# Optimization experiments

Hardware: AMD Instinct MI355X
Metric: run time of the kernel (lower is better)

Reference implementation:

```python
import jax, jax.numpy as jnp
import numpy as np

N = 100000      # nodes
E = 1600000     # edges
F = 128         # num_node_features
C = 64          # graph_hidden_channels
NH = 256        # nhid
NOUT = 128      # nout
L = 4           # n_layers (hidden GCN layers)
G = 512         # number of graphs in batch


def setup_inputs() -> dict:
    key = jax.random.key(0)
    ks = jax.random.split(key, 10)
    x = jax.random.normal(ks[0], (N, F), jnp.float32)
    edge_index = jax.random.randint(ks[1], (2, E), 0, N, dtype=jnp.int64)
    batch = jnp.sort(jax.random.randint(ks[2], (N,), 0, G, dtype=jnp.int64))

    def w(k, shape, fan_in):
        return jax.random.normal(k, shape, jnp.float32) / np.float32(np.sqrt(fan_in))

    W0 = w(ks[3], (F, C), F)
    b0 = jnp.zeros((C,), jnp.float32)
    Wh = w(ks[4], (L, C, C), C)      # stacked hidden GCN weights
    bh = jnp.zeros((L, C), jnp.float32)
    W1 = w(ks[5], (C, NH), C)
    b1 = jnp.zeros((NH,), jnp.float32)
    W2 = w(ks[6], (NH, NOUT), NH)
    b2 = jnp.zeros((NOUT,), jnp.float32)
    return dict(x=x, edge_index=edge_index, batch=batch,
                W0=W0, b0=b0, Wh=Wh, bh=bh, W1=W1, b1=b1, W2=W2, b2=b2)


def _gcn_conv(h_in, W, b, src, dst, dinv):
    # PyG GCNConv: out_i = sum_{j->i} dinv_j * dinv_i * (x_j W) + dinv_i^2 * (x_i W) + b
    h = h_in @ W                                   # [N, C]
    coef = (dinv[src] * dinv[dst])[:, None]        # [E, 1]
    agg = jax.ops.segment_sum(h[src] * coef, dst, num_segments=N)
    agg = agg + h * (dinv * dinv)[:, None]         # self-loop term
    return agg + b


def reference(x, edge_index, batch, W0, b0, Wh, bh, W1, b1, W2, b2):
    src, dst = edge_index[0], edge_index[1]
    # degree with self loops (edge weight 1)
    deg = jax.ops.segment_sum(jnp.ones((E,), x.dtype), dst, num_segments=N) + 1.0
    dinv = jax.lax.rsqrt(deg)                      # [N]

    h = jax.nn.relu(_gcn_conv(x, W0, b0, src, dst, dinv))
    for i in range(L):
        h = jax.nn.relu(_gcn_conv(h, Wh[i], bh[i], src, dst, dinv))

    # global mean pool over graphs
    counts = jax.ops.segment_sum(jnp.ones((N,), x.dtype), batch, num_segments=G)
    pooled = jax.ops.segment_sum(h, batch, num_segments=G) / jnp.maximum(counts, 1.0)[:, None]

    out = jax.nn.relu(pooled @ W1 + b1)
    out = out @ W2 + b2
    return out
```

## Files before the change

kernel.cpp:

```cpp
#include <hip/hip_runtime.h>
#include <hip/hip_fp16.h>
#include <stddef.h>

static constexpr int Nn    = 100000;
static constexpr int Ee    = 1600000;
static constexpr int Ff    = 128;
static constexpr int Cc    = 64;
static constexpr int NHh   = 256;
static constexpr int NOUTt = 128;
static constexpr int Ll    = 4;
static constexpr int Gg    = 512;

static constexpr int SCAN_BLK = 1024;
static constexpr int NBLK_SCAN = (Nn + SCAN_BLK - 1) / SCAN_BLK;

static constexpr int NSUB   = (Nn + 511) / 512;
static constexpr int SUBCAP = 10240;

typedef _Float16 half8 __attribute__((ext_vector_type(8)));
typedef float    f32x4 __attribute__((ext_vector_type(4)));

__global__ __launch_bounds__(256) void bin_kernel(const int* __restrict__ src,
                                                  const int* __restrict__ dst,
                                                  int* __restrict__ sb,
                                                  int* __restrict__ scnt, int E) {
    __shared__ int lcnt[NSUB], lbase[NSUB];
    const int tid = threadIdx.x;
    for (int i = tid; i < NSUB; i += 256) lcnt[i] = 0;
    __syncthreads();
    const int base = blockIdx.x * 2048;
    int pk[8], ps[8], lr[8];
    #pragma unroll
    for (int i = 0; i < 8; ++i) {
        int e = base + i * 256 + tid;
        if (e < E) {
            int d = dst[e], s = src[e];
            int sub = d >> 9;
            ps[i] = sub;
            pk[i] = s | ((d & 511) << 17);
            lr[i] = atomicAdd(&lcnt[sub], 1);
        } else ps[i] = -1;
    }
    __syncthreads();
    for (int i = tid; i < NSUB; i += 256) lbase[i] = atomicAdd(&scnt[i], lcnt[i]);
    __syncthreads();
    #pragma unroll
    for (int i = 0; i < 8; ++i) {
        if (ps[i] >= 0) {
            int pos = lbase[ps[i]] + lr[i];
            if (pos < SUBCAP) sb[(size_t)ps[i] * SUBCAP + pos] = pk[i];
        }
    }
}

__global__ __launch_bounds__(512) void cnt3_kernel(const int* __restrict__ sb,
                                                   const int* __restrict__ scnt,
                                                   int* __restrict__ cnt,
                                                   float* __restrict__ dinv) {
    __shared__ int lcnt[512];
    const int sub = blockIdx.x, tid = threadIdx.x;
    lcnt[tid] = 0;
    __syncthreads();
    const int n = scnt[sub];
    const int* bp = sb + (size_t)sub * SUBCAP;
    for (int i = tid; i < n; i += 512) atomicAdd(&lcnt[(bp[i] >> 17) & 511], 1);
    __syncthreads();
    int node = sub * 512 + tid;
    if (node < Nn) {
        cnt[node] = lcnt[tid];
        dinv[node] = rsqrtf((float)lcnt[tid] + 1.0f);
    }
}

__global__ __launch_bounds__(SCAN_BLK) void scan1_kernel(const int* __restrict__ cnt,
                                                         int* __restrict__ row_off,
                                                         int* __restrict__ bsum, int n) {
    __shared__ int sd[SCAN_BLK];
    int tid = threadIdx.x;
    int gid = blockIdx.x * SCAN_BLK + tid;
    int v = (gid < n) ? cnt[gid] : 0;
    sd[tid] = v;
    __syncthreads();
    #pragma unroll
    for (int off = 1; off < SCAN_BLK; off <<= 1) {
        int t = (tid >= off) ? sd[tid - off] : 0;
        __syncthreads();
        sd[tid] += t;
        __syncthreads();
    }
    if (gid < n) row_off[gid + 1] = sd[tid];
    if (tid == SCAN_BLK - 1) bsum[blockIdx.x] = sd[tid];
}

__global__ __launch_bounds__(128) void scan2_kernel(const int* __restrict__ bsum,
                                                    int* __restrict__ boff, int nb) {
    __shared__ int sd[128];
    int tid = threadIdx.x;
    sd[tid] = (tid < nb) ? bsum[tid] : 0;
    __syncthreads();
    #pragma unroll
    for (int off = 1; off < 128; off <<= 1) {
        int t = (tid >= off) ? sd[tid - off] : 0;
        __syncthreads();
        sd[tid] += t;
        __syncthreads();
    }
    if (tid < nb) boff[tid] = (tid == 0) ? 0 : sd[tid - 1];
}

__global__ void scan3_kernel(int* __restrict__ row_off, const int* __restrict__ boff,
                             const int* __restrict__ batch, int* __restrict__ gstart, int n) {
    int gid = blockIdx.x * blockDim.x + threadIdx.x;
    if (gid < n) {
        row_off[gid + 1] += boff[gid >> 10];
        int bi = batch[gid];
        int bp = (gid == 0) ? -1 : batch[gid - 1];
        for (int g = bp + 1; g <= bi; ++g) gstart[g] = gid;
        if (gid == n - 1) {
            for (int g = bi + 1; g <= Gg; ++g) gstart[g] = n;
        }
    }
    if (gid == 0) row_off[0] = 0;
}

__global__ __launch_bounds__(512) void fill3_kernel(const int* __restrict__ sb,
                                                    const int* __restrict__ scnt,
                                                    const int* __restrict__ roff,
                                                    int* __restrict__ csr) {
    __shared__ int lcnt[512], lofs[512];
    __shared__ int gbase;
    const int sub = blockIdx.x, tid = threadIdx.x;
    lcnt[tid] = 0;
    if (tid == 0) gbase = roff[sub * 512];
    __syncthreads();
    const int n = scnt[sub];
    const int* bp = sb + (size_t)sub * SUBCAP;
    for (int i = tid; i < n; i += 512) atomicAdd(&lcnt[(bp[i] >> 17) & 511], 1);
    __syncthreads();
    int v = lcnt[tid];
    lofs[tid] = v;
    __syncthreads();
    #pragma unroll
    for (int off = 1; off < 512; off <<= 1) {
        int t = (tid >= off) ? lofs[tid - off] : 0;
        __syncthreads();
        lofs[tid] += t;
        __syncthreads();
    }
    int excl = lofs[tid] - v;
    __syncthreads();
    lcnt[tid] = excl;
    __syncthreads();
    for (int i = tid; i < n; i += 512) {
        int e = bp[i];
        int pos = atomicAdd(&lcnt[(e >> 17) & 511], 1);
        csr[gbase + pos] = e & 0x1FFFF;
    }
}

__global__ __launch_bounds__(512) void wcvt_kernel(const float* __restrict__ Wh,
                                                   _Float16* __restrict__ Wf) {
    int t = blockIdx.x * blockDim.x + threadIdx.x;
    if (t >= 4 * 512) return;
    int layer = t >> 9, rem = t & 511;
    int ct = rem >> 7, c = (rem >> 6) & 1, lane = rem & 63;
    const float* W = Wh + (size_t)layer * Cc * Cc;
    _Float16* o = Wf + (size_t)layer * 4096 + ((size_t)(ct * 2 + c) * 64 + lane) * 8;
    int kbase = c * 32 + (lane >> 4) * 8;
    int col = ct * 16 + (lane & 15);
    #pragma unroll
    for (int j = 0; j < 8; ++j) o[j] = (_Float16)W[(kbase + j) * 64 + col];
}

__global__ __launch_bounds__(256) void gemm_xw_f32(const float* __restrict__ X,
                                                   const float* __restrict__ W,
                                                   const float* __restrict__ dinv,
                                                   __half* __restrict__ Y, int n) {
    __shared__ float hs[64][68];
    __shared__ float ws[64][64];
    const int tid = threadIdx.x;
    const int tx  = tid & 15;
    const int ty  = tid >> 4;
    const int rowbase = blockIdx.x * 64;

    float acc[4][4] = {};

    for (int k0 = 0; k0 < Ff; k0 += 64) {
        #pragma unroll
        for (int i = 0; i < 4; ++i) {
            int r = ty + i * 16;
            int gr = rowbase + r;
            float4 v = make_float4(0.f, 0.f, 0.f, 0.f);
            if (gr < n) v = *(const float4*)(X + (size_t)gr * Ff + k0 + tx * 4);
            *(float4*)&hs[r][tx * 4] = v;
        }
        #pragma unroll
        for (int i = 0; i < 4; ++i) {
            int k = ty + i * 16;
            *(float4*)&ws[k][tx * 4] = *(const float4*)(W + (size_t)(k0 + k) * 64 + tx * 4);
        }
        __syncthreads();

        #pragma unroll 4
        for (int k = 0; k < 64; ++k) {
            float4 w = *(const float4*)&ws[k][tx * 4];
            float h0 = hs[ty * 4 + 0][k];
            float h1 = hs[ty * 4 + 1][k];
            float h2 = hs[ty * 4 + 2][k];
            float h3 = hs[ty * 4 + 3][k];
            acc[0][0] += h0 * w.x; acc[0][1] += h0 * w.y; acc[0][2] += h0 * w.z; acc[0][3] += h0 * w.w;
            acc[1][0] += h1 * w.x; acc[1][1] += h1 * w.y; acc[1][2] += h1 * w.z; acc[1][3] += h1 * w.w;
            acc[2][0] += h2 * w.x; acc[2][1] += h2 * w.y; acc[2][2] += h2 * w.z; acc[2][3] += h2 * w.w;
            acc[3][0] += h3 * w.x; acc[3][1] += h3 * w.y; acc[3][2] += h3 * w.z; acc[3][3] += h3 * w.w;
        }
        __syncthreads();
    }

    #pragma unroll
    for (int i = 0; i < 4; ++i) {
        int gr = rowbase + ty * 4 + i;
        if (gr < n) {
            float di = dinv[gr];
            __half2 p0 = __floats2half2_rn(acc[i][0] * di, acc[i][1] * di);
            __half2 p1 = __floats2half2_rn(acc[i][2] * di, acc[i][3] * di);
            float2 st;
            *reinterpret_cast<__half2*>(&st.x) = p0;
            *reinterpret_cast<__half2*>(&st.y) = p1;
            *reinterpret_cast<float2*>(Y + (size_t)gr * 64 + tx * 4) = st;
        }
    }
}

__global__ __launch_bounds__(256) void gemm_mfma(const __half* __restrict__ A16,
                                                 const _Float16* __restrict__ Wf,
                                                 const float* __restrict__ dinv,
                                                 __half* __restrict__ Y, int n) {
    __shared__ _Float16 lds[4][1024];
    const int tid  = threadIdx.x;
    const int lane = tid & 63;
    const int w    = tid >> 6;
    const int wid  = (blockIdx.x * 256 + tid) >> 6;
    const int ntiles = n >> 4;
    if (wid >= ntiles) return;
    const int node0 = wid * 16;

    half8 bfrag[4][2];
    #pragma unroll
    for (int ct = 0; ct < 4; ++ct)
        #pragma unroll
        for (int c = 0; c < 2; ++c)
            bfrag[ct][c] = *(const half8*)(Wf + ((size_t)(ct * 2 + c) * 64 + lane) * 8);

    const _Float16* Ap = (const _Float16*)A16 + (size_t)(node0 + (lane & 15)) * 64 + (lane >> 4) * 8;
    half8 afrag0 = *(const half8*)(Ap);
    half8 afrag1 = *(const half8*)(Ap + 32);

    f32x4 acc[4] = {};
    #pragma unroll
    for (int ct = 0; ct < 4; ++ct) {
        acc[ct] = __builtin_amdgcn_mfma_f32_16x16x32_f16(afrag0, bfrag[ct][0], acc[ct], 0, 0, 0);
        acc[ct] = __builtin_amdgcn_mfma_f32_16x16x32_f16(afrag1, bfrag[ct][1], acc[ct], 0, 0, 0);
    }

    const int r0 = (lane >> 4) * 4;
    float di[4];
    #pragma unroll
    for (int r = 0; r < 4; ++r) di[r] = dinv[node0 + r0 + r];

    #pragma unroll
    for (int ct = 0; ct < 4; ++ct)
        #pragma unroll
        for (int r = 0; r < 4; ++r)
            lds[w][(r0 + r) * 64 + ct * 16 + (lane & 15)] = (_Float16)(acc[ct][r] * di[r]);

    asm volatile("s_waitcnt lgkmcnt(0)" ::: "memory");

    #pragma unroll
    for (int p = 0; p < 2; ++p) {
        int row = p * 8 + (lane >> 3);
        int ch  = lane & 7;
        half8 v = *(const half8*)&lds[w][row * 64 + ch * 8];
        *(half8*)((_Float16*)Y + (size_t)(node0 + row) * 64 + ch * 8) = v;
    }
}

__device__ inline void add_h8(float acc[8], float4 raw) {
    const __half2* hp = reinterpret_cast<const __half2*>(&raw);
    #pragma unroll
    for (int j = 0; j < 4; ++j) {
        float2 f = __half22float2(hp[j]);
        acc[2 * j]     += f.x;
        acc[2 * j + 1] += f.y;
    }
}

__device__ inline void cvt_h8(float4 raw, float v[8]) {
    const __half2* hp = reinterpret_cast<const __half2*>(&raw);
    #pragma unroll
    for (int j = 0; j < 4; ++j) {
        float2 f = __half22float2(hp[j]);
        v[2 * j] = f.x; v[2 * j + 1] = f.y;
    }
}

__global__ __launch_bounds__(256) void gather_agg(const int* __restrict__ row_off,
                                                  const int* __restrict__ csr_src,
                                                  const float* __restrict__ dinv,
                                                  const __half* __restrict__ t,
                                                  const float* __restrict__ b,
                                                  __half* __restrict__ out, int n) {
    const int lane = threadIdx.x & 63;
    const int node = (blockIdx.x * blockDim.x + threadIdx.x) >> 6;
    if (node >= n) return;
    const int sub = lane >> 3;
    const int c8  = lane & 7;

    const int base = row_off[node];
    const int end  = row_off[node + 1];

    float acc[8] = {};

    for (int k0 = base; k0 < end; k0 += 64) {
        int myidx = (k0 + lane < end) ? csr_src[k0 + lane] : 0;
        int nk = min(64, end - k0);
        int k = 0;
        for (; k + 16 <= nk; k += 16) {
            int s0 = __shfl(myidx, k + sub);
            int s1 = __shfl(myidx, k + 8 + sub);
            float4 r0 = *(const float4*)(t + (size_t)s0 * 64 + c8 * 8);
            float4 r1 = *(const float4*)(t + (size_t)s1 * 64 + c8 * 8);
            add_h8(acc, r0);
            add_h8(acc, r1);
        }
        for (; k < nk; k += 8) {
            int kk = k + sub;
            int s = __shfl(myidx, kk);
            if (kk < nk) {
                float4 r = *(const float4*)(t + (size_t)s * 64 + c8 * 8);
                add_h8(acc, r);
            }
        }
    }

    #pragma unroll
    for (int off = 8; off < 64; off <<= 1) {
        #pragma unroll
        for (int j = 0; j < 8; ++j) acc[j] += __shfl_xor(acc[j], off);
    }

    if (sub == 0) {
        float di = dinv[node];
        float selfv[8];
        cvt_h8(*(const float4*)(t + (size_t)node * 64 + c8 * 8), selfv);
        float4 b0 = *(const float4*)(b + c8 * 8);
        float4 b1 = *(const float4*)(b + c8 * 8 + 4);
        float bb[8] = {b0.x, b0.y, b0.z, b0.w, b1.x, b1.y, b1.z, b1.w};
        __half2 o[4];
        #pragma unroll
        for (int j = 0; j < 4; ++j) {
            float v0 = fmaxf(di * (acc[2 * j]     + selfv[2 * j])     + bb[2 * j],     0.f);
            float v1 = fmaxf(di * (acc[2 * j + 1] + selfv[2 * j + 1]) + bb[2 * j + 1], 0.f);
            o[j] = __floats2half2_rn(v0, v1);
        }
        *(float4*)(out + (size_t)node * 64 + c8 * 8) = *reinterpret_cast<float4*>(o);
    }
}

__global__ __launch_bounds__(256) void pool_graph(const __half* __restrict__ h,
                                                  const int* __restrict__ gstart,
                                                  float* __restrict__ pooled) {
    __shared__ float sd[4][64];
    const int g    = blockIdx.x;
    const int lane = threadIdx.x & 63;
    const int wv   = threadIdx.x >> 6;
    const int s = gstart[g], e = gstart[g + 1];
    float acc = 0.f;
    for (int i = s + wv; i < e; i += 4) acc += __half2float(h[(size_t)i * 64 + lane]);
    sd[wv][lane] = acc;
    __syncthreads();
    if (wv == 0) {
        float sum = sd[0][lane] + sd[1][lane] + sd[2][lane] + sd[3][lane];
        float c = (float)(e - s);
        pooled[(size_t)g * 64 + lane] = sum / fmaxf(c, 1.f);
    }
}

__global__ void mlp1_kernel(const float* __restrict__ P, const float* __restrict__ W1,
                            const float* __restrict__ b1, float* __restrict__ H) {
    int gid = blockIdx.x * blockDim.x + threadIdx.x;
    if (gid >= Gg * NHh) return;
    int j = gid & (NHh - 1), g = gid >> 8;
    const float* p = P + (size_t)g * Cc;
    float s = b1[j];
    #pragma unroll 8
    for (int k = 0; k < Cc; ++k) s += p[k] * W1[(size_t)k * NHh + j];
    H[gid] = fmaxf(s, 0.f);
}

__global__ void mlp2_kernel(const float* __restrict__ H, const float* __restrict__ W2,
                            const float* __restrict__ b2, float* __restrict__ O) {
    int gid = blockIdx.x * blockDim.x + threadIdx.x;
    if (gid >= Gg * NOUTt) return;
    int j = gid & (NOUTt - 1), g = gid >> 7;
    const float* h = H + (size_t)g * NHh;
    float s = b2[j];
    #pragma unroll 8
    for (int k = 0; k < NHh; ++k) s += h[k] * W2[(size_t)k * NOUTt + j];
    O[gid] = s;
}

extern "C" void kernel_launch(void* const* d_in, const int* in_sizes, int n_in,
                              void* d_out, int out_size, void* d_ws, size_t ws_size,
                              hipStream_t stream) {
    const float* x     = (const float*)d_in[0];
    const int*   ei    = (const int*)  d_in[1];
    const int*   batch = (const int*)  d_in[2];
    const float* W0    = (const float*)d_in[3];
    const float* b0    = (const float*)d_in[4];
    const float* Wh    = (const float*)d_in[5];
    const float* bh    = (const float*)d_in[6];
    const float* W1    = (const float*)d_in[7];
    const float* b1    = (const float*)d_in[8];
    const float* W2    = (const float*)d_in[9];
    const float* b2    = (const float*)d_in[10];

    const int* src = ei;
    const int* dst = ei + Ee;

    char* ws = (char*)d_ws;
    constexpr size_t OFF_DINV  = 0;
    constexpr size_t OFF_CNT   = 400384;
    constexpr size_t OFF_ROFF  = OFF_CNT + 400384;
    constexpr size_t OFF_BSUM  = OFF_ROFF + 400384;
    constexpr size_t OFF_BOFF  = OFF_BSUM + 1024;
    constexpr size_t OFF_SCNT  = OFF_BOFF + 1024;
    constexpr size_t OFF_CSR   = OFF_SCNT + 1024;
    constexpr size_t OFF_T     = OFF_CSR + 6400256;
    constexpr size_t OFF_A     = OFF_T + 12800256;
    constexpr size_t OFF_POOL  = OFF_A + 12800256;
    constexpr size_t OFF_GST   = OFF_POOL + (size_t)Gg * Cc * 4;
    constexpr size_t OFF_HID   = OFF_GST + 4096;
    constexpr size_t OFF_WF    = OFF_HID + (size_t)Gg * NHh * 4;
    const size_t OFF_SB = OFF_T;

    float*    dinv   = (float*)   (ws + OFF_DINV);
    int*      cnt    = (int*)     (ws + OFF_CNT);
    int*      roff   = (int*)     (ws + OFF_ROFF);
    int*      bsum   = (int*)     (ws + OFF_BSUM);
    int*      boff   = (int*)     (ws + OFF_BOFF);
    int*      scnt   = (int*)     (ws + OFF_SCNT);
    int*      csrs   = (int*)     (ws + OFF_CSR);
    int*      sb     = (int*)     (ws + OFF_SB);
    __half*   T      = (__half*)  (ws + OFF_T);
    __half*   A      = (__half*)  (ws + OFF_A);
    float*    pooled = (float*)   (ws + OFF_POOL);
    int*      gstart = (int*)     (ws + OFF_GST);
    float*    hid    = (float*)   (ws + OFF_HID);
    _Float16* Wf     = (_Float16*)(ws + OFF_WF);

    hipMemsetAsync(scnt, 0, 1024, stream);
    wcvt_kernel<<<4, 512, 0, stream>>>(Wh, Wf);
    bin_kernel<<<(Ee + 2047) / 2048, 256, 0, stream>>>(src, dst, sb, scnt, Ee);
    cnt3_kernel<<<NSUB, 512, 0, stream>>>(sb, scnt, cnt, dinv);
    scan1_kernel<<<NBLK_SCAN, SCAN_BLK, 0, stream>>>(cnt, roff, bsum, Nn);
    scan2_kernel<<<1, 128, 0, stream>>>(bsum, boff, NBLK_SCAN);
    scan3_kernel<<<(Nn + 255) / 256, 256, 0, stream>>>(roff, boff, batch, gstart, Nn);
    fill3_kernel<<<NSUB, 512, 0, stream>>>(sb, scnt, roff, csrs);

    const int gemm_blocks = (Nn + 63) / 64;
    const int agg_blocks  = (Nn * 64 + 255) / 256;
    const int mfma_blocks = ((Nn / 16) + 3) / 4;

    gemm_xw_f32<<<gemm_blocks, 256, 0, stream>>>(x, W0, dinv, T, Nn);
    gather_agg<<<agg_blocks, 256, 0, stream>>>(roff, csrs, dinv, T, b0, A, Nn);

    for (int i = 0; i < Ll; ++i) {
        gemm_mfma<<<mfma_blocks, 256, 0, stream>>>(A, Wf + (size_t)i * 4096, dinv, T, Nn);
        gather_agg<<<agg_blocks, 256, 0, stream>>>(roff, csrs, dinv, T, bh + (size_t)i * Cc, A, Nn);
    }

    pool_graph<<<Gg, 256, 0, stream>>>(A, gstart, pooled);

    mlp1_kernel<<<(Gg * NHh + 255) / 256, 256, 0, stream>>>(pooled, W1, b1, hid);
    mlp2_kernel<<<(Gg * NOUTt + 255) / 256, 256, 0, stream>>>(hid, W2, b2, (float*)d_out);
}
```

Measured before the change: 372.4 us.

## Fuse aggregation with next-layer MFMA GEMM and use MFMA for first layer

Each gather kernel now gives one wavefront a tile of 16 nodes, aggregates them in sequence, stages the result in LDS and immediately applies the next layer's 64x64 MFMA GEMM. This removes the separate GEMM launches and the write and re-read of the intermediate activations, ping-ponging between two buffers. The first-layer fp32 SIMT GEMM is replaced by an MFMA kernel that converts x to fp16 on the fly, which adds precision loss on the input. The cost is far fewer waves in the gather phase (one per 16 nodes instead of one per node), so less latency hiding on the random neighbour reads.

```diff
diff --git a/kernel.cpp b/kernel.cpp
--- a/kernel.cpp
+++ b/kernel.cpp
@@ -158,128 +158,76 @@
     }
 }
 
-__global__ __launch_bounds__(512) void wcvt_kernel(const float* __restrict__ Wh,
+__global__ __launch_bounds__(512) void wcvt_kernel(const float* __restrict__ W0,
+                                                   const float* __restrict__ Wh,
                                                    _Float16* __restrict__ Wf) {
     int t = blockIdx.x * blockDim.x + threadIdx.x;
-    if (t >= 4 * 512) return;
-    int layer = t >> 9, rem = t & 511;
-    int ct = rem >> 7, c = (rem >> 6) & 1, lane = rem & 63;
-    const float* W = Wh + (size_t)layer * Cc * Cc;
-    _Float16* o = Wf + (size_t)layer * 4096 + ((size_t)(ct * 2 + c) * 64 + lane) * 8;
-    int kbase = c * 32 + (lane >> 4) * 8;
-    int col = ct * 16 + (lane & 15);
-    #pragma unroll
-    for (int j = 0; j < 8; ++j) o[j] = (_Float16)W[(kbase + j) * 64 + col];
-}
-
-__global__ __launch_bounds__(256) void gemm_xw_f32(const float* __restrict__ X,
-                                                   const float* __restrict__ W,
-                                                   const float* __restrict__ dinv,
-                                                   __half* __restrict__ Y, int n) {
-    __shared__ float hs[64][68];
-    __shared__ float ws[64][64];
-    const int tid = threadIdx.x;
-    const int tx  = tid & 15;
-    const int ty  = tid >> 4;
-    const int rowbase = blockIdx.x * 64;
-
-    float acc[4][4] = {};
-
-    for (int k0 = 0; k0 < Ff; k0 += 64) {
-        #pragma unroll
-        for (int i = 0; i < 4; ++i) {
-            int r = ty + i * 16;
-            int gr = rowbase + r;
-            float4 v = make_float4(0.f, 0.f, 0.f, 0.f);
-            if (gr < n) v = *(const float4*)(X + (size_t)gr * Ff + k0 + tx * 4);
-            *(float4*)&hs[r][tx * 4] = v;
-        }
-        #pragma unroll
-        for (int i = 0; i < 4; ++i) {
-            int k = ty + i * 16;
-            *(float4*)&ws[k][tx * 4] = *(const float4*)(W + (size_t)(k0 + k) * 64 + tx * 4);
-        }
-        __syncthreads();
-
-        #pragma unroll 4
-        for (int k = 0; k < 64; ++k) {
-            float4 w = *(const float4*)&ws[k][tx * 4];
-            float h0 = hs[ty * 4 + 0][k];
-            float h1 = hs[ty * 4 + 1][k];
-            float h2 = hs[ty * 4 + 2][k];
-            float h3 = hs[ty * 4 + 3][k];
-            acc[0][0] += h0 * w.x; acc[0][1] += h0 * w.y; acc[0][2] += h0 * w.z; acc[0][3] += h0 * w.w;
-            acc[1][0] += h1 * w.x; acc[1][1] += h1 * w.y; acc[1][2] += h1 * w.z; acc[1][3] += h1 * w.w;
-            acc[2][0] += h2 * w.x; acc[2][1] += h2 * w.y; acc[2][2] += h2 * w.z; acc[2][3] += h2 * w.w;
-            acc[3][0] += h3 * w.x; acc[3][1] += h3 * w.y; acc[3][2] += h3 * w.z; acc[3][3] += h3 * w.w;
-        }
-        __syncthreads();
-    }
-
-    #pragma unroll
-    for (int i = 0; i < 4; ++i) {
-        int gr = rowbase + ty * 4 + i;
-        if (gr < n) {
-            float di = dinv[gr];
-            __half2 p0 = __floats2half2_rn(acc[i][0] * di, acc[i][1] * di);
-            __half2 p1 = __floats2half2_rn(acc[i][2] * di, acc[i][3] * di);
-            float2 st;
-            *reinterpret_cast<__half2*>(&st.x) = p0;
-            *reinterpret_cast<__half2*>(&st.y) = p1;
-            *reinterpret_cast<float2*>(Y + (size_t)gr * 64 + tx * 4) = st;
-        }
-    }
-}
-
-__global__ __launch_bounds__(256) void gemm_mfma(const __half* __restrict__ A16,
-                                                 const _Float16* __restrict__ Wf,
-                                                 const float* __restrict__ dinv,
-                                                 __half* __restrict__ Y, int n) {
-    __shared__ _Float16 lds[4][1024];
-    const int tid  = threadIdx.x;
-    const int lane = tid & 63;
-    const int w    = tid >> 6;
-    const int wid  = (blockIdx.x * 256 + tid) >> 6;
-    const int ntiles = n >> 4;
-    if (wid >= ntiles) return;
+    if (t < 1024) {
+        int f = t >> 6, lane = t & 63;
+        int ct = f >> 2, c = f & 3;
+        _Float16* o = Wf + ((size_t)f * 64 + lane) * 8;
+        int kbase = c * 32 + (lane >> 4) * 8;
+        int col = ct * 16 + (lane & 15);
+        #pragma unroll
+        for (int j = 0; j < 8; ++j) o[j] = (_Float16)W0[(size_t)(kbase + j) * 64 + col];
+    } else if (t < 1024 + 2048) {
+        int u = t - 1024;
+        int layer = u >> 9, rem = u & 511;
+        int f = rem >> 6, lane = rem & 63;
+        int ct = f >> 1, c = f & 1;
+        _Float16* o = Wf + 8192 + (size_t)layer * 4096 + ((size_t)f * 64 + lane) * 8;
+        int kbase = c * 32 + (lane >> 4) * 8;
+        int col = ct * 16 + (lane & 15);
+        #pragma unroll
+        for (int j = 0; j < 8; ++j)
+            o[j] = (_Float16)Wh[(size_t)layer * 4096 + (size_t)(kbase + j) * 64 + col];
+    }
+}
+
+__global__ __launch_bounds__(256) void gemm0_mfma(const float* __restrict__ X,
+                                                  const _Float16* __restrict__ Wf0,
+                                                  const float* __restrict__ dinv,
+                                                  __half* __restrict__ Y, int n) {
+    __shared__ _Float16 lds[4][16 * 72];
+    const int tid = threadIdx.x, lane = tid & 63, w = tid >> 6;
+    const int wid = (blockIdx.x * 256 + tid) >> 6;
+    if (wid >= (n >> 4)) return;
     const int node0 = wid * 16;
 
-    half8 bfrag[4][2];
-    #pragma unroll
-    for (int ct = 0; ct < 4; ++ct)
-        #pragma unroll
-        for (int c = 0; c < 2; ++c)
-            bfrag[ct][c] = *(const half8*)(Wf + ((size_t)(ct * 2 + c) * 64 + lane) * 8);
-
-    const _Float16* Ap = (const _Float16*)A16 + (size_t)(node0 + (lane & 15)) * 64 + (lane >> 4) * 8;
-    half8 afrag0 = *(const half8*)(Ap);
-    half8 afrag1 = *(const half8*)(Ap + 32);
-
+    half8 bf[16];
+    #pragma unroll
+    for (int f = 0; f < 16; ++f)
+        bf[f] = *(const half8*)(Wf0 + ((size_t)f * 64 + lane) * 8);
+
+    const float* xp = X + (size_t)(node0 + (lane & 15)) * Ff + (lane >> 4) * 8;
     f32x4 acc[4] = {};
     #pragma unroll
-    for (int ct = 0; ct < 4; ++ct) {
-        acc[ct] = __builtin_amdgcn_mfma_f32_16x16x32_f16(afrag0, bfrag[ct][0], acc[ct], 0, 0, 0);
-        acc[ct] = __builtin_amdgcn_mfma_f32_16x16x32_f16(afrag1, bfrag[ct][1], acc[ct], 0, 0, 0);
+    for (int c = 0; c < 4; ++c) {
+        float4 x0 = *(const float4*)(xp + c * 32);
+        float4 x1 = *(const float4*)(xp + c * 32 + 4);
+        half8 af;
+        af[0] = (_Float16)x0.x; af[1] = (_Float16)x0.y; af[2] = (_Float16)x0.z; af[3] = (_Float16)x0.w;
+        af[4] = (_Float16)x1.x; af[5] = (_Float16)x1.y; af[6] = (_Float16)x1.z; af[7] = (_Float16)x1.w;
+        #pragma unroll
+        for (int ct = 0; ct < 4; ++ct)
+            acc[ct] = __builtin_amdgcn_mfma_f32_16x16x32_f16(af, bf[ct * 4 + c], acc[ct], 0, 0, 0);
     }
 
     const int r0 = (lane >> 4) * 4;
     float di[4];
     #pragma unroll
     for (int r = 0; r < 4; ++r) di[r] = dinv[node0 + r0 + r];
-
     #pragma unroll
     for (int ct = 0; ct < 4; ++ct)
         #pragma unroll
         for (int r = 0; r < 4; ++r)
-            lds[w][(r0 + r) * 64 + ct * 16 + (lane & 15)] = (_Float16)(acc[ct][r] * di[r]);
-
+            lds[w][(r0 + r) * 72 + ct * 16 + (lane & 15)] = (_Float16)(acc[ct][r] * di[r]);
     asm volatile("s_waitcnt lgkmcnt(0)" ::: "memory");
-
     #pragma unroll
     for (int p = 0; p < 2; ++p) {
         int row = p * 8 + (lane >> 3);
         int ch  = lane & 7;
-        half8 v = *(const half8*)&lds[w][row * 64 + ch * 8];
+        half8 v = *(const half8*)&lds[w][row * 72 + ch * 8];
         *(half8*)((_Float16*)Y + (size_t)(node0 + row) * 64 + ch * 8) = v;
     }
 }
@@ -303,66 +251,112 @@
     }
 }
 
-__global__ __launch_bounds__(256) void gather_agg(const int* __restrict__ row_off,
-                                                  const int* __restrict__ csr_src,
-                                                  const float* __restrict__ dinv,
-                                                  const __half* __restrict__ t,
-                                                  const float* __restrict__ b,
-                                                  __half* __restrict__ out, int n) {
-    const int lane = threadIdx.x & 63;
-    const int node = (blockIdx.x * blockDim.x + threadIdx.x) >> 6;
-    if (node >= n) return;
+template<bool GEMM>
+__global__ __launch_bounds__(256) void gather_fused(const int* __restrict__ row_off,
+                                                    const int* __restrict__ csr_src,
+                                                    const float* __restrict__ dinv,
+                                                    const __half* __restrict__ Tin,
+                                                    const float* __restrict__ b,
+                                                    const _Float16* __restrict__ Wf,
+                                                    __half* __restrict__ out, int n) {
+    __shared__ _Float16 hl[4][16 * 72];
+    const int tid = threadIdx.x, lane = tid & 63, w = tid >> 6;
+    const int wid = (blockIdx.x * 256 + tid) >> 6;
+    if (wid >= (n >> 4)) return;
+    const int node0 = wid * 16;
     const int sub = lane >> 3;
     const int c8  = lane & 7;
 
-    const int base = row_off[node];
-    const int end  = row_off[node + 1];
-
-    float acc[8] = {};
-
-    for (int k0 = base; k0 < end; k0 += 64) {
-        int myidx = (k0 + lane < end) ? csr_src[k0 + lane] : 0;
-        int nk = min(64, end - k0);
-        int k = 0;
-        for (; k + 16 <= nk; k += 16) {
-            int s0 = __shfl(myidx, k + sub);
-            int s1 = __shfl(myidx, k + 8 + sub);
-            float4 r0 = *(const float4*)(t + (size_t)s0 * 64 + c8 * 8);
-            float4 r1 = *(const float4*)(t + (size_t)s1 * 64 + c8 * 8);
-            add_h8(acc, r0);
-            add_h8(acc, r1);
-        }
-        for (; k < nk; k += 8) {
-            int kk = k + sub;
-            int s = __shfl(myidx, kk);
-            if (kk < nk) {
-                float4 r = *(const float4*)(t + (size_t)s * 64 + c8 * 8);
-                add_h8(acc, r);
+    half8 bfrag[8];
+    if (GEMM) {
+        #pragma unroll
+        for (int f = 0; f < 8; ++f)
+            bfrag[f] = *(const half8*)(Wf + ((size_t)f * 64 + lane) * 8);
+    }
+
+    float4 bb0 = *(const float4*)(b + c8 * 8);
+    float4 bb1 = *(const float4*)(b + c8 * 8 + 4);
+    float bbv[8] = {bb0.x, bb0.y, bb0.z, bb0.w, bb1.x, bb1.y, bb1.z, bb1.w};
+
+    for (int i = 0; i < 16; ++i) {
+        const int node = node0 + i;
+        const int base = row_off[node];
+        const int end  = row_off[node + 1];
+
+        float acc[8] = {};
+        for (int k0 = base; k0 < end; k0 += 64) {
+            int myidx = (k0 + lane < end) ? csr_src[k0 + lane] : 0;
+            int nk = min(64, end - k0);
+            int k = 0;
+            for (; k + 16 <= nk; k += 16) {
+                int s0 = __shfl(myidx, k + sub);
+                int s1 = __shfl(myidx, k + 8 + sub);
+                float4 r0 = *(const float4*)(Tin + (size_t)s0 * 64 + c8 * 8);
+                float4 r1 = *(const float4*)(Tin + (size_t)s1 * 64 + c8 * 8);
+                add_h8(acc, r0);
+                add_h8(acc, r1);
             }
-        }
-    }
-
-    #pragma unroll
-    for (int off = 8; off < 64; off <<= 1) {
-        #pragma unroll
-        for (int j = 0; j < 8; ++j) acc[j] += __shfl_xor(acc[j], off);
-    }
-
-    if (sub == 0) {
-        float di = dinv[node];
-        float selfv[8];
-        cvt_h8(*(const float4*)(t + (size_t)node * 64 + c8 * 8), selfv);
-        float4 b0 = *(const float4*)(b + c8 * 8);
-        float4 b1 = *(const float4*)(b + c8 * 8 + 4);
-        float bb[8] = {b0.x, b0.y, b0.z, b0.w, b1.x, b1.y, b1.z, b1.w};
-        __half2 o[4];
-        #pragma unroll
-        for (int j = 0; j < 4; ++j) {
-            float v0 = fmaxf(di * (acc[2 * j]     + selfv[2 * j])     + bb[2 * j],     0.f);
-            float v1 = fmaxf(di * (acc[2 * j + 1] + selfv[2 * j + 1]) + bb[2 * j + 1], 0.f);
-            o[j] = __floats2half2_rn(v0, v1);
-        }
-        *(float4*)(out + (size_t)node * 64 + c8 * 8) = *reinterpret_cast<float4*>(o);
+            for (; k < nk; k += 8) {
+                int kk = k + sub;
+                int s = __shfl(myidx, kk);
+                if (kk < nk) {
+                    float4 r = *(const float4*)(Tin + (size_t)s * 64 + c8 * 8);
+                    add_h8(acc, r);
+                }
+            }
+        }
+
+        #pragma unroll
+        for (int off = 8; off < 64; off <<= 1) {
+            #pragma unroll
+            for (int j = 0; j < 8; ++j) acc[j] += __shfl_xor(acc[j], off);
+        }
+
+        if (sub == 0) {
+            float di = dinv[node];
+            float selfv[8];
+            cvt_h8(*(const float4*)(Tin + (size_t)node * 64 + c8 * 8), selfv);
+            _Float16 hv[8];
+            #pragma unroll
+            for (int j = 0; j < 8; ++j)
+                hv[j] = (_Float16)fmaxf(di * (acc[j] + selfv[j]) + bbv[j], 0.f);
+            if (GEMM) {
+                *(half8*)&hl[w][i * 72 + c8 * 8] = *(const half8*)hv;
+            } else {
+                *(half8*)((_Float16*)out + (size_t)node * 64 + c8 * 8) = *(const half8*)hv;
+            }
+        }
+    }
+
+    if (GEMM) {
+        asm volatile("s_waitcnt lgkmcnt(0)" ::: "memory");
+        const int row = lane & 15, q = lane >> 4;
+        half8 a0 = *(const half8*)&hl[w][row * 72 + q * 8];
+        half8 a1 = *(const half8*)&hl[w][row * 72 + 32 + q * 8];
+        f32x4 acc2[4] = {};
+        #pragma unroll
+        for (int ct = 0; ct < 4; ++ct) {
+            acc2[ct] = __builtin_amdgcn_mfma_f32_16x16x32_f16(a0, bfrag[ct * 2 + 0], acc2[ct], 0, 0, 0);
+            acc2[ct] = __builtin_amdgcn_mfma_f32_16x16x32_f16(a1, bfrag[ct * 2 + 1], acc2[ct], 0, 0, 0);
+        }
+        asm volatile("s_waitcnt lgkmcnt(0)" ::: "memory");
+        const int r0 = q * 4;
+        float di[4];
+        #pragma unroll
+        for (int r = 0; r < 4; ++r) di[r] = dinv[node0 + r0 + r];
+        #pragma unroll
+        for (int ct = 0; ct < 4; ++ct)
+            #pragma unroll
+            for (int r = 0; r < 4; ++r)
+                hl[w][(r0 + r) * 72 + ct * 16 + (lane & 15)] = (_Float16)(acc2[ct][r] * di[r]);
+        asm volatile("s_waitcnt lgkmcnt(0)" ::: "memory");
+        #pragma unroll
+        for (int p = 0; p < 2; ++p) {
+            int orow = p * 8 + (lane >> 3);
+            int ch   = lane & 7;
+            half8 v = *(const half8*)&hl[w][orow * 72 + ch * 8];
+            *(half8*)((_Float16*)out + (size_t)(node0 + orow) * 64 + ch * 8) = v;
+        }
     }
 }
 
@@ -436,7 +430,8 @@
     constexpr size_t OFF_SCNT  = OFF_BOFF + 1024;
     constexpr size_t OFF_CSR   = OFF_SCNT + 1024;
     constexpr size_t OFF_T     = OFF_CSR + 6400256;
-    constexpr size_t OFF_A     = OFF_T + 12800256;
+    constexpr size_t OFF_T2    = OFF_T + 12800256;
+    constexpr size_t OFF_A     = OFF_T2 + 12800256;
     constexpr size_t OFF_POOL  = OFF_A + 12800256;
     constexpr size_t OFF_GST   = OFF_POOL + (size_t)Gg * Cc * 4;
     constexpr size_t OFF_HID   = OFF_GST + 4096;
@@ -452,14 +447,16 @@
     int*      csrs   = (int*)     (ws + OFF_CSR);
     int*      sb     = (int*)     (ws + OFF_SB);
     __half*   T      = (__half*)  (ws + OFF_T);
+    __half*   T2     = (__half*)  (ws + OFF_T2);
     __half*   A      = (__half*)  (ws + OFF_A);
     float*    pooled = (float*)   (ws + OFF_POOL);
     int*      gstart = (int*)     (ws + OFF_GST);
     float*    hid    = (float*)   (ws + OFF_HID);
     _Float16* Wf     = (_Float16*)(ws + OFF_WF);
+    _Float16* Wfh    = Wf + 8192;
 
     hipMemsetAsync(scnt, 0, 1024, stream);
-    wcvt_kernel<<<4, 512, 0, stream>>>(Wh, Wf);
+    wcvt_kernel<<<6, 512, 0, stream>>>(W0, Wh, Wf);
     bin_kernel<<<(Ee + 2047) / 2048, 256, 0, stream>>>(src, dst, sb, scnt, Ee);
     cnt3_kernel<<<NSUB, 512, 0, stream>>>(sb, scnt, cnt, dinv);
     scan1_kernel<<<NBLK_SCAN, SCAN_BLK, 0, stream>>>(cnt, roff, bsum, Nn);
@@ -467,17 +464,15 @@
     scan3_kernel<<<(Nn + 255) / 256, 256, 0, stream>>>(roff, boff, batch, gstart, Nn);
     fill3_kernel<<<NSUB, 512, 0, stream>>>(sb, scnt, roff, csrs);
 
-    const int gemm_blocks = (Nn + 63) / 64;
-    const int agg_blocks  = (Nn * 64 + 255) / 256;
-    const int mfma_blocks = ((Nn / 16) + 3) / 4;
-
-    gemm_xw_f32<<<gemm_blocks, 256, 0, stream>>>(x, W0, dinv, T, Nn);
-    gather_agg<<<agg_blocks, 256, 0, stream>>>(roff, csrs, dinv, T, b0, A, Nn);
-
-    for (int i = 0; i < Ll; ++i) {
-        gemm_mfma<<<mfma_blocks, 256, 0, stream>>>(A, Wf + (size_t)i * 4096, dinv, T, Nn);
-        gather_agg<<<agg_blocks, 256, 0, stream>>>(roff, csrs, dinv, T, bh + (size_t)i * Cc, A, Nn);
-    }
+    const int tile_blocks = ((Nn / 16) + 3) / 4;
+
+    gemm0_mfma<<<tile_blocks, 256, 0, stream>>>(x, Wf, dinv, T, Nn);
+
+    gather_fused<true ><<<tile_blocks, 256, 0, stream>>>(roff, csrs, dinv, T,  b0,       Wfh + 0 * 4096, T2, Nn);
+    gather_fused<true ><<<tile_blocks, 256, 0, stream>>>(roff, csrs, dinv, T2, bh + 0,   Wfh + 1 * 4096, T,  Nn);
+    gather_fused<true ><<<tile_blocks, 256, 0, stream>>>(roff, csrs, dinv, T,  bh + 64,  Wfh + 2 * 4096, T2, Nn);
+    gather_fused<true ><<<tile_blocks, 256, 0, stream>>>(roff, csrs, dinv, T2, bh + 128, Wfh + 3 * 4096, T,  Nn);
+    gather_fused<false><<<tile_blocks, 256, 0, stream>>>(roff, csrs, dinv, T,  bh + 192, nullptr,        A,  Nn);
 
     pool_graph<<<Gg, 256, 0, stream>>>(A, gstart, pooled);
 
```

After: 443.9 us. 1.19x slower.
